# Kernel optimization log

Measured on AMD Instinct MI355X. Metric: run time of the kernel, lower is better.

The kernel has to match this reference:

```python
import jax, jax.numpy as jnp
import numpy as np

B = 2048          # batch (vmapped samples)
STEPS = 64        # hardcoded scan length in module
H = 64            # hidden_size
W = 128           # width_size
NZ = 32           # noise_size (control_size)
INZ = 32          # initial_noise_size
D = 8             # data_size


def lipswish(x):
    return 0.909 * jax.nn.silu(x)


def _mlp3(x, W0, b0, W1, b1, W2, b2, act, final_act):
    # eqx.nn.MLP with depth=2: in->width, width->width, width->out
    h = act(x @ W0.T + b0)
    h = act(h @ W1.T + b1)
    return final_act(h @ W2.T + b2)


def setup_inputs() -> dict:
    key = jax.random.key(0)
    ks = jax.random.split(key, 32)

    def lin(k, out_d, in_d):
        lim = 1.0 / np.sqrt(in_d)
        kw, kb = jax.random.split(k)
        Wm = jax.random.uniform(kw, (out_d, in_d), minval=-lim, maxval=lim, dtype=jnp.float32)
        bv = jax.random.uniform(kb, (out_d,), minval=-lim, maxval=lim, dtype=jnp.float32)
        return Wm, bv

    Wi0, bi0 = lin(ks[0], W, INZ)
    Wi1, bi1 = lin(ks[1], W, W)
    Wi2, bi2 = lin(ks[2], H, W)

    Wv0, bv0 = lin(ks[3], W, H + 1)
    Wv1, bv1 = lin(ks[4], W, W)
    Wv2, bv2 = lin(ks[5], H, W)
    scale_v = jax.random.uniform(ks[6], (H,), minval=0.9, maxval=1.1, dtype=jnp.float32)

    Wc0, bc0 = lin(ks[7], W, H + 1)
    Wc1, bc1 = lin(ks[8], W, W)
    Wc2, bc2 = lin(ks[9], H * NZ, W)
    scale_c = jax.random.uniform(ks[10], (H, NZ), minval=0.9, maxval=1.1, dtype=jnp.float32)

    Wr, br = lin(ks[11], D, H)

    ts = jnp.arange(STEPS + 1, dtype=jnp.float32)
    init_noise = jax.random.normal(ks[12], (B, INZ), dtype=jnp.float32)
    bm = jax.random.normal(ks[13], (B, STEPS, NZ), dtype=jnp.float32)

    return dict(ts=ts, init_noise=init_noise, bm=bm,
                Wi0=Wi0, bi0=bi0, Wi1=Wi1, bi1=bi1, Wi2=Wi2, bi2=bi2,
                scale_v=scale_v, Wv0=Wv0, bv0=bv0, Wv1=Wv1, bv1=bv1, Wv2=Wv2, bv2=bv2,
                scale_c=scale_c, Wc0=Wc0, bc0=bc0, Wc1=Wc1, bc1=bc1, Wc2=Wc2, bc2=bc2,
                Wr=Wr, br=br)


def reference(ts, init_noise, bm,
              Wi0, bi0, Wi1, bi1, Wi2, bi2,
              scale_v, Wv0, bv0, Wv1, bv1, Wv2, bv2,
              scale_c, Wc0, bc0, Wc1, bc1, Wc2, bc2,
              Wr, br):
    t0 = ts[0]
    dt = jnp.float32(1.0)  # dt0 hardcoded in module
    sqrt_dt = jnp.sqrt(dt)

    # initial MLP (relu hidden, identity final): noise -> y0 [B,H]
    y0 = _mlp3(init_noise, Wi0, bi0, Wi1, bi1, Wi2, bi2, jax.nn.relu, lambda x: x)

    bm_t = jnp.transpose(bm, (1, 0, 2))  # [STEPS, B, NZ]
    idx = jnp.arange(STEPS, dtype=jnp.float32)

    def step(y, xs):
        i, bm_i = xs
        t = t0 + i * dt
        tcol = jnp.broadcast_to(jnp.reshape(t, (1, 1)), (y.shape[0], 1))
        inp = jnp.concatenate([tcol, y], axis=1)  # [B, H+1]
        # drift vector field
        drift = scale_v * _mlp3(inp, Wv0, bv0, Wv1, bv1, Wv2, bv2, lipswish, jnp.tanh)
        # controlled vector field: [B, H, NZ]
        diff = scale_c * _mlp3(inp, Wc0, bc0, Wc1, bc1, Wc2, bc2, lipswish, jnp.tanh).reshape(-1, H, NZ)
        y1 = y + drift * dt + jnp.einsum('bhn,bn->bh', diff, bm_i * sqrt_dt)
        return y1, y1

    _, ys = jax.lax.scan(step, y0, (idx, bm_t), length=STEPS, unroll=8)  # ys [STEPS,B,H]
    out = jnp.einsum('tbh,dh->tbd', ys, Wr) + br  # readout per step
    return jnp.transpose(out, (1, 0, 2))  # [B, STEPS, D]
```

## Files before the change

kernel.cpp:

```cpp
#include <hip/hip_runtime.h>
#include <stdint.h>
#include <stddef.h>


typedef __attribute__((ext_vector_type(8))) short bf16x8;
typedef __attribute__((ext_vector_type(4))) float f32x4;
typedef __attribute__((ext_vector_type(4))) int   i32x4;

#define BB 16
#define NWG 256

#define WS_WI0 0
#define WS_WI1 8192
#define WS_WI2 40960
#define WS_WV0 57344
#define WS_WV1 73728
#define WS_WV2 106496
#define WS_WC0 122880
#define WS_WC1 139264
#define WS_WC2 172032
#define WS_TV0 696320
#define WS_TC0 696832
#define WS_XCHG 700416
#define WS_FLAG 2273280

#define LD_WV0 0
#define LD_WV1 16384
#define LD_WC0 49152
#define LD_WC1 65536
#define LD_YBF 98304
#define LD_H1V 100352
#define LD_H1C 104448
#define LD_H2V 108544
#define LD_H2C 112640
#define LD_Y   116736
#define LD_DB  121088
#define LD_BM  125440
#define LD_BSC 127552
#define LD_BEV 135744
#define LD_BEC 136256
#define LD_BV1 136768
#define LD_BC1 137280
#define LD_BV2 137792
#define LD_SV  138048
#define LD_WR  138304
#define LD_BR  140480
#define LD_WV2 140512
#define LDS_TOTAL 148704

__device__ __forceinline__ short f2bf(float f) {
  uint32_t u = __builtin_bit_cast(uint32_t, f);
  uint32_t r = (u + 0x7fffu + ((u >> 16) & 1u)) >> 16;
  return (short)r;
}
__device__ __forceinline__ float bf2f(short s) {
  uint32_t u = ((uint32_t)(uint16_t)s) << 16;
  return __builtin_bit_cast(float, u);
}
__device__ __forceinline__ float tanh_fast(float x) {
  float e = __builtin_amdgcn_exp2f(x * 2.8853900817779268f);
  return __builtin_fmaf(-2.f, __builtin_amdgcn_rcpf(e + 1.f), 1.f);
}
__device__ __forceinline__ float lipswish(float x) {
  float s = __builtin_amdgcn_rcpf(1.f + __builtin_amdgcn_exp2f(-1.4426950408889634f * x));
  return 0.909f * x * s;
}
__device__ __forceinline__ float red16(float x) {
  int v;
  v = __builtin_amdgcn_update_dpp(0, __builtin_bit_cast(int, x), 0xB1, 0xF, 0xF, true);
  x += __builtin_bit_cast(float, v);
  v = __builtin_amdgcn_update_dpp(0, __builtin_bit_cast(int, x), 0x4E, 0xF, 0xF, true);
  x += __builtin_bit_cast(float, v);
  v = __builtin_amdgcn_update_dpp(0, __builtin_bit_cast(int, x), 0x141, 0xF, 0xF, true);
  x += __builtin_bit_cast(float, v);
  v = __builtin_amdgcn_update_dpp(0, __builtin_bit_cast(int, x), 0x140, 0xF, 0xF, true);
  x += __builtin_bit_cast(float, v);
  return x;
}
__device__ __forceinline__ float red4(float x) {
  int v;
  v = __builtin_amdgcn_update_dpp(0, __builtin_bit_cast(int, x), 0xB1, 0xF, 0xF, true);
  x += __builtin_bit_cast(float, v);
  v = __builtin_amdgcn_update_dpp(0, __builtin_bit_cast(int, x), 0x4E, 0xF, 0xF, true);
  x += __builtin_bit_cast(float, v);
  return x;
}
__device__ __forceinline__ void write_act(char* buf, int m, int k, short v) {
  int addr = ((k >> 5) << 10) + (m + ((k >> 3) & 3) * 16) * 16 + ((k & 7) << 1);
  *(short*)(buf + addr) = v;
}

template<int KF>
__device__ __forceinline__ f32x4 gemm_tile(const char* abase, const char* bbase, int lane) {
  f32x4 acc = {0.f, 0.f, 0.f, 0.f};
#pragma unroll
  for (int k = 0; k < KF; k++) {
    bf16x8 a = *(const bf16x8*)(abase + k * 1024 + lane * 16);
    bf16x8 b = *(const bf16x8*)(bbase + k * 1024 + lane * 16);
    acc = __builtin_amdgcn_mfma_f32_16x16x32_bf16(a, b, acc, 0, 0, 0);
  }
  return acc;
}

__global__ __launch_bounds__(256) void prep_kernel(
    const float* Wi0, const float* Wi1, const float* Wi2,
    const float* Wv0, const float* Wv1, const float* Wv2,
    const float* Wc0, const float* Wc1, const float* Wc2, char* ws) {
  int gid = blockIdx.x * 256 + threadIdx.x;
  if (gid < 512) ((unsigned*)(ws + WS_FLAG))[gid] = 0;
  if (gid < 680 * 64) {
    int frag = gid >> 6, lane = gid & 63;
    const float* src; int start, KI, srcK, c0;
    if      (frag < 8)   { src = Wi0; start = 0;   KI = 1; srcK = 32;  c0 = 0; }
    else if (frag < 40)  { src = Wi1; start = 8;   KI = 4; srcK = 128; c0 = 0; }
    else if (frag < 56)  { src = Wi2; start = 40;  KI = 4; srcK = 128; c0 = 0; }
    else if (frag < 72)  { src = Wv0; start = 56;  KI = 2; srcK = 65;  c0 = 1; }
    else if (frag < 104) { src = Wv1; start = 72;  KI = 4; srcK = 128; c0 = 0; }
    else if (frag < 120) { src = Wv2; start = 104; KI = 4; srcK = 128; c0 = 0; }
    else if (frag < 136) { src = Wc0; start = 120; KI = 2; srcK = 65;  c0 = 1; }
    else if (frag < 168) { src = Wc1; start = 136; KI = 4; srcK = 128; c0 = 0; }
    else                 { src = Wc2; start = 168; KI = 4; srcK = 128; c0 = 0; }
    int rel = frag - start;
    int nt = rel / KI, ki = rel % KI;
    int n16 = lane & 15, quad = lane >> 4;
    const float* s = src + (nt * 16 + n16) * srcK + c0 + ki * 32 + quad * 8;
    bf16x8 v;
#pragma unroll
    for (int j = 0; j < 8; j++) v[j] = f2bf(s[j]);
    *(bf16x8*)(ws + (size_t)frag * 1024 + lane * 16) = v;
  } else {
    int i = gid - 680 * 64;
    if (i < 128)      ((float*)(ws + WS_TV0))[i] = Wv0[i * 65];
    else if (i < 256) ((float*)(ws + WS_TC0))[i - 128] = Wc0[(i - 128) * 65];
  }
}

__global__ __launch_bounds__(512, 2)
void sde_kernel(
    const float* ts, const float* init_noise, const float* bm,
    const float* bi0, const float* bi1, const float* bi2,
    const float* bv0, const float* bv1, const float* bv2, const float* scale_v,
    const float* bc0, const float* bc1, const float* bc2, const float* scale_c,
    const float* Wr, const float* br,
    char* ws, float* out) {
  extern __shared__ __align__(16) char lds[];
  const int tid  = threadIdx.x;
  const int lane = tid & 63;
  const int wv   = tid >> 6;
  const int nl   = lane & 15;
  const int quad = lane >> 4;
  const int bid  = blockIdx.x;
  const int ro   = (bid >> 3) & 1;
  const int pid  = ((bid >> 4) << 3) | (bid & 7);
  const int b0   = pid * BB;
  const int hbase = ro << 5;
  const char* wc2 = ws + WS_WC2 + (size_t)(ro * 64 + wv * 8) * 4096;
  char* xch = ws + WS_XCHG;
  unsigned* flags = (unsigned*)(ws + WS_FLAG);
  const int myflag = (pid << 1) | ro;
  const int paflag = (pid << 1) | (1 - ro);
  const float brv = (tid < 128) ? br[tid & 7] : 0.f;

  float tvq = 0.f, bbq = 0.f;
  if (tid >= 256) {
    int j = tid - 256;
    if (j < 128) { tvq = ((const float*)(ws + WS_TV0))[j];       bbq = bv0[j]; }
    else         { tvq = ((const float*)(ws + WS_TC0))[j - 128]; bbq = bc0[j - 128]; }
  }

  {
    const i32x4* s0 = (const i32x4*)(ws + WS_WV0);
    const i32x4* s1 = (const i32x4*)(ws + WS_WC0);
    i32x4* d0 = (i32x4*)(lds + LD_WV0);
    i32x4* d1 = (i32x4*)(lds + LD_WC0);
    for (int j = tid; j < 3072; j += 512) { d0[j] = s0[j]; d1[j] = s1[j]; }
  }
  {
    const i32x4* s2 = (const i32x4*)(ws + WS_WV2 + ro * 8192);
    ((i32x4*)(lds + LD_WV2))[tid] = s2[tid];
  }
  for (int j = tid; j < 2048; j += 512) {
    uint32_t u = (uint32_t)(uint16_t)f2bf(bc2[j]) |
                 ((uint32_t)(uint16_t)f2bf(scale_c[j]) << 16);
    ((uint32_t*)(lds + LD_BSC))[j] = u;
  }
  if (tid < 128)      { ((float*)(lds + LD_BV1))[tid] = bv1[tid];
                        ((float*)(lds + LD_BC1))[tid] = bc1[tid]; }
  else if (tid < 192) { int k = tid - 128; ((float*)(lds + LD_BV2))[k] = bv2[k];
                        ((float*)(lds + LD_SV))[k] = scale_v[k]; }
  else if (tid < 200) { int k = tid - 192; ((float*)(lds + LD_BR))[k] = br[k]; }
  { int dd = tid >> 6, k = tid & 63;
    ((float*)(lds + LD_WR))[dd * 68 + k] = Wr[dd * 64 + k]; }
  { int m = tid >> 5, k = tid & 31;
    write_act(lds + LD_YBF, m, k, f2bf(init_noise[(b0 + m) * 32 + k])); }
  __syncthreads();

  { f32x4 acc = gemm_tile<1>(lds + LD_YBF, ws + WS_WI0 + wv * 1024, lane);
    int col = wv * 16 + nl; float bias = bi0[col];
#pragma unroll
    for (int r = 0; r < 4; r++)
      write_act(lds + LD_H1V, quad * 4 + r, col, f2bf(fmaxf(0.f, acc[r] + bias))); }
  __syncthreads();
  { f32x4 acc = gemm_tile<4>(lds + LD_H1V, ws + WS_WI1 + wv * 4096, lane);
    int col = wv * 16 + nl; float bias = bi1[col];
#pragma unroll
    for (int r = 0; r < 4; r++)
      write_act(lds + LD_H2V, quad * 4 + r, col, f2bf(fmaxf(0.f, acc[r] + bias))); }
  __syncthreads();
  if (wv < 4) {
    f32x4 acc = gemm_tile<4>(lds + LD_H2V, ws + WS_WI2 + wv * 4096, lane);
    int col = wv * 16 + nl; float bias = bi2[col];
#pragma unroll
    for (int r = 0; r < 4; r++)
      ((float*)(lds + LD_Y))[(quad * 4 + r) * 68 + col] = acc[r] + bias;
  }
  __syncthreads();

#define LOADT(N, OFF)                                                          \
  bf16x8 w##N##a = *(const bf16x8*)(wc2 + (OFF) +    0 + lane * 16);           \
  bf16x8 w##N##b = *(const bf16x8*)(wc2 + (OFF) + 1024 + lane * 16);           \
  bf16x8 w##N##c = *(const bf16x8*)(wc2 + (OFF) + 2048 + lane * 16);           \
  bf16x8 w##N##d = *(const bf16x8*)(wc2 + (OFF) + 3072 + lane * 16);
  LOADT(0, 0)     LOADT(1, 4096)  LOADT(2, 8192)  LOADT(3, 12288)
  LOADT(4, 16384) LOADT(5, 20480) LOADT(6, 24576) LOADT(7, 28672)
#undef LOADT

  const float ts0 = ts[0];
  for (int e = tid; e < 1024; e += 512) {
    int row = e >> 6, k = e & 63;
    write_act(lds + LD_YBF, row, k, f2bf(((float*)(lds + LD_Y))[row * 68 + k]));
  }
  ((float*)(lds + LD_BM))[(tid >> 5) * 33 + (tid & 31)] =
      bm[((size_t)(b0 + (tid >> 5)) * 64 + 0) * 32 + (tid & 31)];
  if (tid >= 256) {
    int j = tid - 256; float v = bbq + ts0 * tvq;
    if (j < 128) ((float*)(lds + LD_BEV))[j] = v;
    else         ((float*)(lds + LD_BEC))[j - 128] = v;
  }
  __syncthreads();

  for (int step = 0; step < 64; step++) {
    {
      int col = wv * 16 + nl;
      f32x4 av = gemm_tile<2>(lds + LD_YBF, lds + LD_WV0 + wv * 2048, lane);
      f32x4 ac = gemm_tile<2>(lds + LD_YBF, lds + LD_WC0 + wv * 2048, lane);
      float bv = ((float*)(lds + LD_BEV))[col];
      float bc = ((float*)(lds + LD_BEC))[col];
#pragma unroll
      for (int r = 0; r < 4; r++) {
        write_act(lds + LD_H1V, quad * 4 + r, col, f2bf(lipswish(av[r] + bv)));
        write_act(lds + LD_H1C, quad * 4 + r, col, f2bf(lipswish(ac[r] + bc)));
      }
    }
    __syncthreads();
    {
      int col = wv * 16 + nl;
      f32x4 av = gemm_tile<4>(lds + LD_H1V, lds + LD_WV1 + wv * 4096, lane);
      f32x4 ac = gemm_tile<4>(lds + LD_H1C, lds + LD_WC1 + wv * 4096, lane);
      float bv = ((float*)(lds + LD_BV1))[col];
      float bc = ((float*)(lds + LD_BC1))[col];
#pragma unroll
      for (int r = 0; r < 4; r++) {
        write_act(lds + LD_H2V, quad * 4 + r, col, f2bf(lipswish(av[r] + bv)));
        write_act(lds + LD_H2C, quad * 4 + r, col, f2bf(lipswish(ac[r] + bc)));
      }
    }
    __syncthreads();
    float bm_next = 0.f;
    if (step + 1 < 64)
      bm_next = bm[((size_t)(b0 + (tid >> 5)) * 64 + (step + 1)) * 32 + (tid & 31)];
    if (wv < 2) {
      const char* vb = lds + LD_WV2 + wv * 4096;
      f32x4 acc = {0.f, 0.f, 0.f, 0.f};
      acc = __builtin_amdgcn_mfma_f32_16x16x32_bf16(
          *(const bf16x8*)(lds + LD_H2V +    0 + lane * 16),
          *(const bf16x8*)(vb +    0 + lane * 16), acc, 0, 0, 0);
      acc = __builtin_amdgcn_mfma_f32_16x16x32_bf16(
          *(const bf16x8*)(lds + LD_H2V + 1024 + lane * 16),
          *(const bf16x8*)(vb + 1024 + lane * 16), acc, 0, 0, 0);
      acc = __builtin_amdgcn_mfma_f32_16x16x32_bf16(
          *(const bf16x8*)(lds + LD_H2V + 2048 + lane * 16),
          *(const bf16x8*)(vb + 2048 + lane * 16), acc, 0, 0, 0);
      acc = __builtin_amdgcn_mfma_f32_16x16x32_bf16(
          *(const bf16x8*)(lds + LD_H2V + 3072 + lane * 16),
          *(const bf16x8*)(vb + 3072 + lane * 16), acc, 0, 0, 0);
      int col = (ro * 2 + wv) * 16 + nl;
      float bias = ((float*)(lds + LD_BV2))[col];
      float sv   = ((float*)(lds + LD_SV))[col];
#pragma unroll
      for (int r = 0; r < 4; r++)
        ((float*)(lds + LD_DB))[(quad * 4 + r) * 68 + col] = sv * tanh_fast(acc[r] + bias);
    }
    {
      bf16x8 a0f = *(const bf16x8*)(lds + LD_H2C +    0 + lane * 16);
      bf16x8 a1f = *(const bf16x8*)(lds + LD_H2C + 1024 + lane * 16);
      bf16x8 a2f = *(const bf16x8*)(lds + LD_H2C + 2048 + lane * 16);
      bf16x8 a3f = *(const bf16x8*)(lds + LD_H2C + 3072 + lane * 16);
      const float* bmp = (const float*)(lds + LD_BM);
      float bmr00 = bmp[(quad * 4 + 0) * 33 + nl];
      float bmr01 = bmp[(quad * 4 + 1) * 33 + nl];
      float bmr02 = bmp[(quad * 4 + 2) * 33 + nl];
      float bmr03 = bmp[(quad * 4 + 3) * 33 + nl];
      float bmr10 = bmp[(quad * 4 + 0) * 33 + 16 + nl];
      float bmr11 = bmp[(quad * 4 + 1) * 33 + 16 + nl];
      float bmr12 = bmp[(quad * 4 + 2) * 33 + 16 + nl];
      float bmr13 = bmp[(quad * 4 + 3) * 33 + 16 + nl];
      const uint32_t* bscp = (const uint32_t*)(lds + LD_BSC) + (ro * 64 + wv * 8) * 16 + nl;
      float ps0, ps1, ps2, ps3;

#define DIFF_PAIR(P, E0, E1, E2, E3, O0, O1, O2, O3)                          \
      {                                                     \
        f32x4 acc = {0.f, 0.f, 0.f, 0.f};                                     \
        acc = __builtin_amdgcn_mfma_f32_16x16x32_bf16(a0f, E0, acc, 0, 0, 0); \
        acc = __builtin_amdgcn_mfma_f32_16x16x32_bf16(a1f, E1, acc, 0, 0, 0); \
        acc = __builtin_amdgcn_mfma_f32_16x16x32_bf16(a2f, E2, acc, 0, 0, 0); \
        acc = __builtin_amdgcn_mfma_f32_16x16x32_bf16(a3f, E3, acc, 0, 0, 0); \
        uint32_t bsc = bscp[(2*(P))*16];                                      \
        float bc2v = bf2f((short)(bsc & 0xffffu));                            \
        float scv  = bf2f((short)(bsc >> 16));                                \
        ps0 = tanh_fast(acc[0] + bc2v) * scv * bmr00;                         \
        ps1 = tanh_fast(acc[1] + bc2v) * scv * bmr01;                         \
        ps2 = tanh_fast(acc[2] + bc2v) * scv * bmr02;                         \
        ps3 = tanh_fast(acc[3] + bc2v) * scv * bmr03;                         \
      }                                                                       \
      {                                                    \
        f32x4 acc = {0.f, 0.f, 0.f, 0.f};                                     \
        acc = __builtin_amdgcn_mfma_f32_16x16x32_bf16(a0f, O0, acc, 0, 0, 0); \
        acc = __builtin_amdgcn_mfma_f32_16x16x32_bf16(a1f, O1, acc, 0, 0, 0); \
        acc = __builtin_amdgcn_mfma_f32_16x16x32_bf16(a2f, O2, acc, 0, 0, 0); \
        acc = __builtin_amdgcn_mfma_f32_16x16x32_bf16(a3f, O3, acc, 0, 0, 0); \
        uint32_t bsc = bscp[(2*(P)+1)*16];                                    \
        float bc2v = bf2f((short)(bsc & 0xffffu));                            \
        float scv  = bf2f((short)(bsc >> 16));                                \
        ps0 += tanh_fast(acc[0] + bc2v) * scv * bmr10;                        \
        ps1 += tanh_fast(acc[1] + bc2v) * scv * bmr11;                        \
        ps2 += tanh_fast(acc[2] + bc2v) * scv * bmr12;                        \
        ps3 += tanh_fast(acc[3] + bc2v) * scv * bmr13;                        \
        ps0 = red16(ps0); ps1 = red16(ps1); ps2 = red16(ps2); ps3 = red16(ps3);\
        if (nl < 4) {                                                         \
          int row = quad * 4 + nl;                                            \
          float s = (nl == 0) ? ps0 : (nl == 1) ? ps1 : (nl == 2) ? ps2 : ps3;\
          ((float*)(lds + LD_Y))[row * 68 + (hbase + (wv << 2) + (P))] += s;  \
        }                                                                     \
      }

      DIFF_PAIR(0, w0a, w0b, w0c, w0d, w1a, w1b, w1c, w1d)
      DIFF_PAIR(1, w2a, w2b, w2c, w2d, w3a, w3b, w3c, w3d)
      DIFF_PAIR(2, w4a, w4b, w4c, w4d, w5a, w5b, w5c, w5d)
      DIFF_PAIR(3, w6a, w6b, w6c, w6d, w7a, w7b, w7c, w7d)
#undef DIFF_PAIR
    }
    __syncthreads();
    char* my_slot = xch + (size_t)(((myflag << 1) | (step & 1))) * 2048;
    const char* pa_slot = xch + (size_t)(((paflag << 1) | (step & 1))) * 2048;
    float part = 0.f;
    if (tid < 128) {
      int row = tid >> 3, kq = tid & 7;
      int c0 = hbase + kq * 4;
      f32x4 yv = *(const f32x4*)(lds + LD_Y  + (row * 68 + c0) * 4);
      f32x4 db = *(const f32x4*)(lds + LD_DB + (row * 68 + c0) * 4);
      f32x4 vn = yv + db;
      *(f32x4*)(lds + LD_Y + (row * 68 + c0) * 4) = vn;
      uint32_t p0 = (uint32_t)(uint16_t)f2bf(vn[0]) | ((uint32_t)(uint16_t)f2bf(vn[1]) << 16);
      uint32_t p1 = (uint32_t)(uint16_t)f2bf(vn[2]) | ((uint32_t)(uint16_t)f2bf(vn[3]) << 16);
      uint64_t p64 = (uint64_t)p0 | ((uint64_t)p1 << 32);
      int inner = (row + (kq >> 1) * 16) * 16 + ((kq & 1) << 3);
      *(uint64_t*)(lds + LD_YBF + ro * 1024 + inner) = p64;
      __hip_atomic_store((unsigned long long*)(my_slot + inner), (unsigned long long)p64,
                         __ATOMIC_RELAXED, __HIP_MEMORY_SCOPE_AGENT);
      const float* yr = (const float*)(lds + LD_Y) + row * 68 + hbase;
      const float* wr = (const float*)(lds + LD_WR) + kq * 68 + hbase;
#pragma unroll
      for (int j = 0; j < 8; j++) {
        f32x4 a = *(const f32x4*)(yr + j * 4);
        f32x4 w = *(const f32x4*)(wr + j * 4);
        part = fmaf(a[0], w[0], part); part = fmaf(a[1], w[1], part);
        part = fmaf(a[2], w[2], part); part = fmaf(a[3], w[3], part);
      }
      if ((tid >> 6) != ro)
        __hip_atomic_store((unsigned*)(my_slot + 1024) + (tid & 63),
                           __builtin_bit_cast(unsigned, part),
                           __ATOMIC_RELAXED, __HIP_MEMORY_SCOPE_AGENT);
      asm volatile("s_waitcnt vmcnt(0)" ::: "memory");
      if (lane == 0)
        __hip_atomic_store(flags + ((myflag << 1) | (tid >> 6)), (unsigned)(step + 1),
                           __ATOMIC_RELAXED, __HIP_MEMORY_SCOPE_AGENT);
    } else if (tid >= 256 && step + 1 < 64) {
      int j = tid - 256; float v = bbq + (ts0 + (float)(step + 1)) * tvq;
      if (j < 128) ((float*)(lds + LD_BEV))[j] = v;
      else         ((float*)(lds + LD_BEC))[j - 128] = v;
    }
    if (step + 1 < 64)
      ((float*)(lds + LD_BM))[(tid >> 5) * 33 + (tid & 31)] = bm_next;
    if (tid < 128) {
      unsigned want = (unsigned)(step + 1);
      const unsigned long long* pfl = (const unsigned long long*)(flags + (paflag << 1));
      int guard = 0;
      for (;;) {
        unsigned long long fv = __hip_atomic_load(pfl, __ATOMIC_RELAXED,
                                                  __HIP_MEMORY_SCOPE_AGENT);
        if ((unsigned)fv >= want && (unsigned)(fv >> 32) >= want) break;
        __builtin_amdgcn_s_sleep(1);
        if (++guard > (1 << 20)) break;
      }
      unsigned long long v = __hip_atomic_load((const unsigned long long*)pa_slot + tid,
                                               __ATOMIC_RELAXED, __HIP_MEMORY_SCOPE_AGENT);
      *(unsigned long long*)(lds + LD_YBF + (1 - ro) * 1024 + tid * 8) = v;
      if ((tid >> 6) == ro) {
        float pp = __builtin_bit_cast(float, __hip_atomic_load(
            (const unsigned*)(pa_slot + 1024) + (tid & 63),
            __ATOMIC_RELAXED, __HIP_MEMORY_SCOPE_AGENT));
        int row = tid >> 3, dd = tid & 7;
        out[(size_t)(b0 + row) * 512 + step * 8 + dd] = part + pp + brv;
      }
    }
    __syncthreads();
  }
}

extern "C" void kernel_launch(void* const* d_in, const int* in_sizes, int n_in,
                              void* d_out, int out_size, void* d_ws, size_t ws_size,
                              hipStream_t stream) {
  (void)in_sizes; (void)n_in; (void)out_size; (void)ws_size;
  const float* ts         = (const float*)d_in[0];
  const float* init_noise = (const float*)d_in[1];
  const float* bm         = (const float*)d_in[2];
  const float* Wi0 = (const float*)d_in[3];
  const float* bi0 = (const float*)d_in[4];
  const float* Wi1 = (const float*)d_in[5];
  const float* bi1 = (const float*)d_in[6];
  const float* Wi2 = (const float*)d_in[7];
  const float* bi2 = (const float*)d_in[8];
  const float* scale_v = (const float*)d_in[9];
  const float* Wv0 = (const float*)d_in[10];
  const float* bv0 = (const float*)d_in[11];
  const float* Wv1 = (const float*)d_in[12];
  const float* bv1 = (const float*)d_in[13];
  const float* Wv2 = (const float*)d_in[14];
  const float* bv2 = (const float*)d_in[15];
  const float* scale_c = (const float*)d_in[16];
  const float* Wc0 = (const float*)d_in[17];
  const float* bc0 = (const float*)d_in[18];
  const float* Wc1 = (const float*)d_in[19];
  const float* bc1 = (const float*)d_in[20];
  const float* Wc2 = (const float*)d_in[21];
  const float* bc2 = (const float*)d_in[22];
  const float* Wr  = (const float*)d_in[23];
  const float* br  = (const float*)d_in[24];
  char*  ws  = (char*)d_ws;
  float* out = (float*)d_out;

  hipFuncSetAttribute((const void*)sde_kernel,
                      hipFuncAttributeMaxDynamicSharedMemorySize, LDS_TOTAL);

  prep_kernel<<<171, 256, 0, stream>>>(Wi0, Wi1, Wi2, Wv0, Wv1, Wv2, Wc0, Wc1, Wc2, ws);
  sde_kernel<<<NWG, 512, LDS_TOTAL, stream>>>(
      ts, init_noise, bm, bi0, bi1, bi2, bv0, bv1, bv2, scale_v,
      bc0, bc1, bc2, scale_c, Wr, br, ws, out);
}
```

Before: 448.0 us.

## Publish y state to partner block per wave right after diffusion, split flags

Moves the y update, bf16 packing and cross-workgroup exchange store out of the post-barrier section into each diffusion wave, gated by an LDS flag set once the drift wave has written its slice. Each wave now posts its own global flag, and the partner waits on eight wave flags plus a separate flag for the readout partial sums. This lets the exchange data leave earlier instead of waiting for the full block barrier, shortening the per-step critical path between paired blocks. It also swaps the manual bf16 rounding for the packed hardware convert instruction. The cost is more flag traffic, an LDS spin-wait inside waves, and more complex memory-ordering assumptions.

```diff
diff --git a/kernel.cpp b/kernel.cpp
--- a/kernel.cpp
+++ b/kernel.cpp
@@ -46,7 +46,8 @@
 #define LD_WR  138304
 #define LD_BR  140480
 #define LD_WV2 140512
-#define LDS_TOTAL 148704
+#define LD_DFL 148704
+#define LDS_TOTAL 148712
 
 __device__ __forceinline__ short f2bf(float f) {
   uint32_t u = __builtin_bit_cast(uint32_t, f);
@@ -56,6 +57,11 @@
 __device__ __forceinline__ float bf2f(short s) {
   uint32_t u = ((uint32_t)(uint16_t)s) << 16;
   return __builtin_bit_cast(float, u);
+}
+__device__ __forceinline__ uint32_t cvtpk(float lo, float hi) {
+  uint32_t r;
+  asm("v_cvt_pk_bf16_f32 %0, %1, %2" : "=v"(r) : "v"(lo), "v"(hi));
+  return r;
 }
 __device__ __forceinline__ float tanh_fast(float x) {
   float e = __builtin_amdgcn_exp2f(x * 2.8853900817779268f);
@@ -77,14 +83,6 @@
   x += __builtin_bit_cast(float, v);
   return x;
 }
-__device__ __forceinline__ float red4(float x) {
-  int v;
-  v = __builtin_amdgcn_update_dpp(0, __builtin_bit_cast(int, x), 0xB1, 0xF, 0xF, true);
-  x += __builtin_bit_cast(float, v);
-  v = __builtin_amdgcn_update_dpp(0, __builtin_bit_cast(int, x), 0x4E, 0xF, 0xF, true);
-  x += __builtin_bit_cast(float, v);
-  return x;
-}
 __device__ __forceinline__ void write_act(char* buf, int m, int k, short v) {
   int addr = ((k >> 5) << 10) + (m + ((k >> 3) & 3) * 16) * 16 + ((k & 7) << 1);
   *(short*)(buf + addr) = v;
@@ -107,7 +105,7 @@
     const float* Wv0, const float* Wv1, const float* Wv2,
     const float* Wc0, const float* Wc1, const float* Wc2, char* ws) {
   int gid = blockIdx.x * 256 + threadIdx.x;
-  if (gid < 512) ((unsigned*)(ws + WS_FLAG))[gid] = 0;
+  if (gid < 4096) ((unsigned*)(ws + WS_FLAG))[gid] = 0;
   if (gid < 680 * 64) {
     int frag = gid >> 6, lane = gid & 63;
     const float* src; int start, KI, srcK, c0;
@@ -184,6 +182,7 @@
                  ((uint32_t)(uint16_t)f2bf(scale_c[j]) << 16);
     ((uint32_t*)(lds + LD_BSC))[j] = u;
   }
+  if (tid < 2) ((unsigned*)(lds + LD_DFL))[tid] = 0;
   if (tid < 128)      { ((float*)(lds + LD_BV1))[tid] = bv1[tid];
                         ((float*)(lds + LD_BC1))[tid] = bc1[tid]; }
   else if (tid < 192) { int k = tid - 128; ((float*)(lds + LD_BV2))[k] = bv2[k];
@@ -240,17 +239,27 @@
   __syncthreads();
 
   for (int step = 0; step < 64; step++) {
+    char* my_slot = xch + (size_t)(((myflag << 1) | (step & 1))) * 2048;
+    const char* pa_slot = xch + (size_t)(((paflag << 1) | (step & 1))) * 2048;
+    const unsigned want = (unsigned)(step + 1);
     {
       int col = wv * 16 + nl;
       f32x4 av = gemm_tile<2>(lds + LD_YBF, lds + LD_WV0 + wv * 2048, lane);
       f32x4 ac = gemm_tile<2>(lds + LD_YBF, lds + LD_WC0 + wv * 2048, lane);
       float bv = ((float*)(lds + LD_BEV))[col];
       float bc = ((float*)(lds + LD_BEC))[col];
-#pragma unroll
-      for (int r = 0; r < 4; r++) {
-        write_act(lds + LD_H1V, quad * 4 + r, col, f2bf(lipswish(av[r] + bv)));
-        write_act(lds + LD_H1C, quad * 4 + r, col, f2bf(lipswish(ac[r] + bc)));
-      }
+      uint32_t p0 = cvtpk(lipswish(av[0] + bv), lipswish(av[1] + bv));
+      uint32_t p1 = cvtpk(lipswish(av[2] + bv), lipswish(av[3] + bv));
+      uint32_t q0 = cvtpk(lipswish(ac[0] + bc), lipswish(ac[1] + bc));
+      uint32_t q1 = cvtpk(lipswish(ac[2] + bc), lipswish(ac[3] + bc));
+      write_act(lds + LD_H1V, quad * 4 + 0, col, (short)p0);
+      write_act(lds + LD_H1V, quad * 4 + 1, col, (short)(p0 >> 16));
+      write_act(lds + LD_H1V, quad * 4 + 2, col, (short)p1);
+      write_act(lds + LD_H1V, quad * 4 + 3, col, (short)(p1 >> 16));
+      write_act(lds + LD_H1C, quad * 4 + 0, col, (short)q0);
+      write_act(lds + LD_H1C, quad * 4 + 1, col, (short)(q0 >> 16));
+      write_act(lds + LD_H1C, quad * 4 + 2, col, (short)q1);
+      write_act(lds + LD_H1C, quad * 4 + 3, col, (short)(q1 >> 16));
     }
     __syncthreads();
     {
@@ -259,11 +268,18 @@
       f32x4 ac = gemm_tile<4>(lds + LD_H1C, lds + LD_WC1 + wv * 4096, lane);
       float bv = ((float*)(lds + LD_BV1))[col];
       float bc = ((float*)(lds + LD_BC1))[col];
-#pragma unroll
-      for (int r = 0; r < 4; r++) {
-        write_act(lds + LD_H2V, quad * 4 + r, col, f2bf(lipswish(av[r] + bv)));
-        write_act(lds + LD_H2C, quad * 4 + r, col, f2bf(lipswish(ac[r] + bc)));
-      }
+      uint32_t p0 = cvtpk(lipswish(av[0] + bv), lipswish(av[1] + bv));
+      uint32_t p1 = cvtpk(lipswish(av[2] + bv), lipswish(av[3] + bv));
+      uint32_t q0 = cvtpk(lipswish(ac[0] + bc), lipswish(ac[1] + bc));
+      uint32_t q1 = cvtpk(lipswish(ac[2] + bc), lipswish(ac[3] + bc));
+      write_act(lds + LD_H2V, quad * 4 + 0, col, (short)p0);
+      write_act(lds + LD_H2V, quad * 4 + 1, col, (short)(p0 >> 16));
+      write_act(lds + LD_H2V, quad * 4 + 2, col, (short)p1);
+      write_act(lds + LD_H2V, quad * 4 + 3, col, (short)(p1 >> 16));
+      write_act(lds + LD_H2C, quad * 4 + 0, col, (short)q0);
+      write_act(lds + LD_H2C, quad * 4 + 1, col, (short)(q0 >> 16));
+      write_act(lds + LD_H2C, quad * 4 + 2, col, (short)q1);
+      write_act(lds + LD_H2C, quad * 4 + 3, col, (short)(q1 >> 16));
     }
     __syncthreads();
     float bm_next = 0.f;
@@ -290,6 +306,8 @@
 #pragma unroll
       for (int r = 0; r < 4; r++)
         ((float*)(lds + LD_DB))[(quad * 4 + r) * 68 + col] = sv * tanh_fast(acc[r] + bias);
+      asm volatile("s_waitcnt lgkmcnt(0)" ::: "memory");
+      if (lane == 0) ((unsigned*)(lds + LD_DFL))[wv] = want;
     }
     {
       bf16x8 a0f = *(const bf16x8*)(lds + LD_H2C +    0 + lane * 16);
@@ -323,6 +341,7 @@
         ps2 = tanh_fast(acc[2] + bc2v) * scv * bmr02;                         \
         ps3 = tanh_fast(acc[3] + bc2v) * scv * bmr03;                         \
       }                                                                       \
+      float s##P;                                                             \
       {                                                    \
         f32x4 acc = {0.f, 0.f, 0.f, 0.f};                                     \
         acc = __builtin_amdgcn_mfma_f32_16x16x32_bf16(a0f, O0, acc, 0, 0, 0); \
@@ -337,11 +356,7 @@
         ps2 += tanh_fast(acc[2] + bc2v) * scv * bmr12;                        \
         ps3 += tanh_fast(acc[3] + bc2v) * scv * bmr13;                        \
         ps0 = red16(ps0); ps1 = red16(ps1); ps2 = red16(ps2); ps3 = red16(ps3);\
-        if (nl < 4) {                                                         \
-          int row = quad * 4 + nl;                                            \
-          float s = (nl == 0) ? ps0 : (nl == 1) ? ps1 : (nl == 2) ? ps2 : ps3;\
-          ((float*)(lds + LD_Y))[row * 68 + (hbase + (wv << 2) + (P))] += s;  \
-        }                                                                     \
+        s##P = (nl == 0) ? ps0 : (nl == 1) ? ps1 : (nl == 2) ? ps2 : ps3;     \
       }
 
       DIFF_PAIR(0, w0a, w0b, w0c, w0d, w1a, w1b, w1c, w1d)
@@ -349,25 +364,42 @@
       DIFF_PAIR(2, w4a, w4b, w4c, w4d, w5a, w5b, w5c, w5d)
       DIFF_PAIR(3, w6a, w6b, w6c, w6d, w7a, w7b, w7c, w7d)
 #undef DIFF_PAIR
+
+      {
+        volatile unsigned* df = (volatile unsigned*)(lds + LD_DFL) + (wv >> 2);
+        int g = 0;
+        while (*df < want) { __builtin_amdgcn_s_sleep(0); if (++g > (1 << 20)) break; }
+        __builtin_amdgcn_sched_barrier(0);
+        if (nl < 4) {
+          int row = quad * 4 + nl;
+          int c0 = hbase + (wv << 2);
+          f32x4 yv = *(const f32x4*)(lds + LD_Y  + (row * 68 + c0) * 4);
+          f32x4 db = *(const f32x4*)(lds + LD_DB + (row * 68 + c0) * 4);
+          f32x4 vn;
+          vn[0] = (yv[0] + s0) + db[0];
+          vn[1] = (yv[1] + s1) + db[1];
+          vn[2] = (yv[2] + s2) + db[2];
+          vn[3] = (yv[3] + s3) + db[3];
+          *(f32x4*)(lds + LD_Y + (row * 68 + c0) * 4) = vn;
+          uint32_t lo = cvtpk(vn[0], vn[1]);
+          uint32_t hi = cvtpk(vn[2], vn[3]);
+          uint64_t p64 = (uint64_t)lo | ((uint64_t)hi << 32);
+          int inner = (row + (wv >> 1) * 16) * 16 + ((wv & 1) << 3);
+          *(uint64_t*)(lds + LD_YBF + ro * 1024 + inner) = p64;
+          __hip_atomic_store((unsigned long long*)(my_slot + inner),
+                             (unsigned long long)p64,
+                             __ATOMIC_RELAXED, __HIP_MEMORY_SCOPE_AGENT);
+        }
+        asm volatile("s_waitcnt vmcnt(0)" ::: "memory");
+        if (lane == 0)
+          __hip_atomic_store(flags + myflag * 16 + wv, want,
+                             __ATOMIC_RELAXED, __HIP_MEMORY_SCOPE_AGENT);
+      }
     }
     __syncthreads();
-    char* my_slot = xch + (size_t)(((myflag << 1) | (step & 1))) * 2048;
-    const char* pa_slot = xch + (size_t)(((paflag << 1) | (step & 1))) * 2048;
     float part = 0.f;
     if (tid < 128) {
       int row = tid >> 3, kq = tid & 7;
-      int c0 = hbase + kq * 4;
-      f32x4 yv = *(const f32x4*)(lds + LD_Y  + (row * 68 + c0) * 4);
-      f32x4 db = *(const f32x4*)(lds + LD_DB + (row * 68 + c0) * 4);
-      f32x4 vn = yv + db;
-      *(f32x4*)(lds + LD_Y + (row * 68 + c0) * 4) = vn;
-      uint32_t p0 = (uint32_t)(uint16_t)f2bf(vn[0]) | ((uint32_t)(uint16_t)f2bf(vn[1]) << 16);
-      uint32_t p1 = (uint32_t)(uint16_t)f2bf(vn[2]) | ((uint32_t)(uint16_t)f2bf(vn[3]) << 16);
-      uint64_t p64 = (uint64_t)p0 | ((uint64_t)p1 << 32);
-      int inner = (row + (kq >> 1) * 16) * 16 + ((kq & 1) << 3);
-      *(uint64_t*)(lds + LD_YBF + ro * 1024 + inner) = p64;
-      __hip_atomic_store((unsigned long long*)(my_slot + inner), (unsigned long long)p64,
-                         __ATOMIC_RELAXED, __HIP_MEMORY_SCOPE_AGENT);
       const float* yr = (const float*)(lds + LD_Y) + row * 68 + hbase;
       const float* wr = (const float*)(lds + LD_WR) + kq * 68 + hbase;
 #pragma unroll
@@ -383,7 +415,7 @@
                            __ATOMIC_RELAXED, __HIP_MEMORY_SCOPE_AGENT);
       asm volatile("s_waitcnt vmcnt(0)" ::: "memory");
       if (lane == 0)
-        __hip_atomic_store(flags + ((myflag << 1) | (tid >> 6)), (unsigned)(step + 1),
+        __hip_atomic_store(flags + myflag * 16 + 8 + (tid >> 6), want,
                            __ATOMIC_RELAXED, __HIP_MEMORY_SCOPE_AGENT);
     } else if (tid >= 256 && step + 1 < 64) {
       int j = tid - 256; float v = bbq + (ts0 + (float)(step + 1)) * tvq;
@@ -393,20 +425,31 @@
     if (step + 1 < 64)
       ((float*)(lds + LD_BM))[(tid >> 5) * 33 + (tid & 31)] = bm_next;
     if (tid < 128) {
-      unsigned want = (unsigned)(step + 1);
-      const unsigned long long* pfl = (const unsigned long long*)(flags + (paflag << 1));
-      int guard = 0;
+      const unsigned long long* sf = (const unsigned long long*)(flags + paflag * 16);
+      int g = 0;
       for (;;) {
-        unsigned long long fv = __hip_atomic_load(pfl, __ATOMIC_RELAXED,
-                                                  __HIP_MEMORY_SCOPE_AGENT);
-        if ((unsigned)fv >= want && (unsigned)(fv >> 32) >= want) break;
+        unsigned long long f0 = __hip_atomic_load(sf + 0, __ATOMIC_RELAXED, __HIP_MEMORY_SCOPE_AGENT);
+        unsigned long long f1 = __hip_atomic_load(sf + 1, __ATOMIC_RELAXED, __HIP_MEMORY_SCOPE_AGENT);
+        unsigned long long f2 = __hip_atomic_load(sf + 2, __ATOMIC_RELAXED, __HIP_MEMORY_SCOPE_AGENT);
+        unsigned long long f3 = __hip_atomic_load(sf + 3, __ATOMIC_RELAXED, __HIP_MEMORY_SCOPE_AGENT);
+        if ((unsigned)f0 >= want && (unsigned)(f0 >> 32) >= want &&
+            (unsigned)f1 >= want && (unsigned)(f1 >> 32) >= want &&
+            (unsigned)f2 >= want && (unsigned)(f2 >> 32) >= want &&
+            (unsigned)f3 >= want && (unsigned)(f3 >> 32) >= want) break;
         __builtin_amdgcn_s_sleep(1);
-        if (++guard > (1 << 20)) break;
+        if (++g > (1 << 20)) break;
       }
       unsigned long long v = __hip_atomic_load((const unsigned long long*)pa_slot + tid,
                                                __ATOMIC_RELAXED, __HIP_MEMORY_SCOPE_AGENT);
       *(unsigned long long*)(lds + LD_YBF + (1 - ro) * 1024 + tid * 8) = v;
       if ((tid >> 6) == ro) {
+        int g2 = 0;
+        for (;;) {
+          unsigned long long fp = __hip_atomic_load(sf + 4, __ATOMIC_RELAXED, __HIP_MEMORY_SCOPE_AGENT);
+          if ((unsigned)fp >= want && (unsigned)(fp >> 32) >= want) break;
+          __builtin_amdgcn_s_sleep(1);
+          if (++g2 > (1 << 20)) break;
+        }
         float pp = __builtin_bit_cast(float, __hip_atomic_load(
             (const unsigned*)(pa_slot + 1024) + (tid & 63),
             __ATOMIC_RELAXED, __HIP_MEMORY_SCOPE_AGENT));
```

New measurement: 461.0 us. 2.9% more time.
